# Optimization experiments

Hardware: AMD Instinct MI355X
Metric: run time of the kernel (lower is better)

The kernel has to match this reference:

```python
import jax, jax.numpy as jnp
import numpy as np

B, S, D = 2, 2048, 4096
H, KVH, HD = 32, 8, 128
MULT = 0.08838834764831845  # 1/sqrt(head_dim)
MAXV = 30.0                 # tanh soft-cap
ROPE_BASE = 10000.0


def _rope_cos_sin(position_ids, hd=HD, base=ROPE_BASE):
    inv_freq = 1.0 / (base ** (jnp.arange(0, hd, 2, dtype=jnp.float32) / hd))
    freqs = position_ids.astype(jnp.float32)[..., None] * inv_freq  # [B,S,hd/2]
    emb = jnp.concatenate([freqs, freqs], axis=-1)                  # [B,S,hd]
    return jnp.cos(emb), jnp.sin(emb)


def _rotate_half(x):
    half = x.shape[-1] // 2
    return jnp.concatenate([-x[..., half:], x[..., :half]], axis=-1)


def setup_inputs() -> dict:
    key = jax.random.key(0)
    ks = jax.random.split(key, 5)
    hidden_states = jax.random.normal(ks[0], (B, S, D), dtype=jnp.float32)
    position_ids = jnp.broadcast_to(jnp.arange(S, dtype=jnp.int64), (B, S))
    # True = masked (causal upper triangle)
    causal = jnp.triu(jnp.ones((S, S), dtype=bool), k=1)
    attention_mask = jnp.broadcast_to(causal, (B, 1, S, S))
    sc = 0.02
    q_w = jax.random.normal(ks[1], (D, H * HD), dtype=jnp.float32) * sc
    k_w = jax.random.normal(ks[2], (D, KVH * HD), dtype=jnp.float32) * sc
    v_w = jax.random.normal(ks[3], (D, KVH * HD), dtype=jnp.float32) * sc
    o_w = jax.random.normal(ks[4], (H * HD, D), dtype=jnp.float32) * sc
    return {"hidden_states": hidden_states, "position_ids": position_ids,
            "attention_mask": attention_mask, "q_w": q_w, "k_w": k_w,
            "v_w": v_w, "o_w": o_w}


def reference(hidden_states, position_ids, attention_mask, q_w, k_w, v_w, o_w):
    bsz, q_len, _ = hidden_states.shape
    q = (hidden_states @ q_w).reshape(bsz, q_len, H, HD).transpose(0, 2, 1, 3)    # [B,H,S,HD]
    k = (hidden_states @ k_w).reshape(bsz, q_len, KVH, HD).transpose(0, 2, 1, 3)  # [B,KVH,S,HD]
    v = (hidden_states @ v_w).reshape(bsz, q_len, KVH, HD).transpose(0, 2, 1, 3)

    cos, sin = _rope_cos_sin(position_ids)   # [B,S,HD]
    cos = cos[:, None]                       # [B,1,S,HD]
    sin = sin[:, None]
    q = q * cos + _rotate_half(q) * sin
    k = k * cos + _rotate_half(k) * sin

    groups = H // KVH
    k = jnp.repeat(k, groups, axis=1)        # [B,H,S,HD]
    v = jnp.repeat(v, groups, axis=1)

    scores = jnp.einsum('bhqd,bhkd->bhqk', q, k).astype(jnp.float32) * MULT
    scores = MAXV * jnp.tanh(scores / MAXV)
    scores = jnp.where(attention_mask, jnp.float32(-10000.0), scores)
    attn = jax.nn.softmax(scores, axis=-1).astype(q.dtype)

    out = jnp.einsum('bhqk,bhkd->bhqd', attn, v)       # [B,H,S,HD]
    out = out.transpose(0, 2, 1, 3).reshape(bsz, q_len, H * HD)
    return out @ o_w
```

## Files before the change

### kernel.cpp

```cpp
#include <hip/hip_runtime.h>
#include <stdint.h>

#define B_ 2
#define S_ 2048
#define D_ 4096
#define H_ 32
#define KVH_ 8
#define HD_ 128
#define GRP_ (H_/KVH_)
#define NQKV 6144
#define MULT_ 0.08838834764831845f
#define MAXV_ 30.0f

typedef __attribute__((ext_vector_type(8))) short s16x8;
typedef __attribute__((ext_vector_type(4))) float fx4;

__device__ __forceinline__ unsigned short f2bf(float f) {
  unsigned int u = __float_as_uint(f);
  u += 0x7fffu + ((u >> 16) & 1u);
  return (unsigned short)(u >> 16);
}
__device__ __forceinline__ float bf2f(unsigned short h) {
  return __uint_as_float(((unsigned int)h) << 16);
}

__device__ __forceinline__ void gld_lds16(const void* g, void* l) {
  __builtin_amdgcn_global_load_lds(
      (const __attribute__((address_space(1))) unsigned int*)g,
      (__attribute__((address_space(3))) unsigned int*)l, 16, 0, 0);
}


__global__ void k_f2bf(const float* __restrict__ src, unsigned short* __restrict__ dst, int n4) {
  int i = blockIdx.x * blockDim.x + threadIdx.x;
  int stride = gridDim.x * blockDim.x;
  for (; i < n4; i += stride) {
    float4 v = ((const float4*)src)[i];
    ushort4 o;
    o.x = f2bf(v.x); o.y = f2bf(v.y); o.z = f2bf(v.z); o.w = f2bf(v.w);
    ((ushort4*)dst)[i] = o;
  }
}

__global__ void k_transpose_w(const float* __restrict__ src, int ncols,
                              unsigned short* __restrict__ dst) {
  __shared__ float tile[32][33];
  int k0 = blockIdx.x * 32;
  int n0 = blockIdx.y * 32;
  int tx = threadIdx.x, ty = threadIdx.y;
  for (int i = 0; i < 32; i += 8)
    tile[ty + i][tx] = src[(size_t)(k0 + ty + i) * ncols + n0 + tx];
  __syncthreads();
  for (int i = 0; i < 32; i += 8)
    dst[(size_t)(n0 + ty + i) * 4096 + k0 + tx] = f2bf(tile[tx][ty + i]);
}

__global__ void k_transpose_v(const unsigned short* __restrict__ qkv,
                              unsigned short* __restrict__ vt) {
  __shared__ unsigned short tile[32][33];
  int s0 = blockIdx.x * 32;
  int d0 = blockIdx.y * 32;
  int bk = blockIdx.z;
  int b = bk / KVH_, kvh = bk % KVH_;
  int tx = threadIdx.x, ty = threadIdx.y;
  for (int i = 0; i < 32; i += 8)
    tile[ty + i][tx] = qkv[(size_t)(b*S_ + s0 + ty + i)*NQKV + 5120 + kvh*HD_ + d0 + tx];
  __syncthreads();
  for (int i = 0; i < 32; i += 8)
    vt[((size_t)bk*HD_ + d0 + ty + i)*S_ + s0 + tx] = tile[tx][ty + i];
}

__global__ void k_rope(const unsigned short* __restrict__ qkv,
                       unsigned short* __restrict__ Q, unsigned short* __restrict__ K) {
  int bs = blockIdx.x;
  int b = bs >> 11;
  int s = bs & (S_ - 1);
  __shared__ float cs[64], sn[64];
  int t = threadIdx.x;
  if (t < 64) {
    float inv = __expf(-(float)t * 0.14391156831212787f);
    float fr = (float)s * inv;
    cs[t] = cosf(fr); sn[t] = sinf(fr);
  }
  __syncthreads();
  const unsigned short* row = qkv + (size_t)bs * NQKV;
  for (int i = t; i < H_*HD_; i += 256) {
    int h = i >> 7, d = i & 127;
    float x = bf2f(row[i]);
    float x2, c, si;
    if (d < 64) { x2 = -bf2f(row[h*128 + d + 64]); c = cs[d];    si = sn[d]; }
    else        { x2 =  bf2f(row[h*128 + d - 64]); c = cs[d-64]; si = sn[d-64]; }
    Q[((size_t)(b*H_ + h)*S_ + s)*HD_ + d] = f2bf(x*c + x2*si);
  }
  for (int i = t; i < KVH_*HD_; i += 256) {
    int h = i >> 7, d = i & 127;
    float x = bf2f(row[4096 + i]);
    float x2, c, si;
    if (d < 64) { x2 = -bf2f(row[4096 + h*128 + d + 64]); c = cs[d];    si = sn[d]; }
    else        { x2 =  bf2f(row[4096 + h*128 + d - 64]); c = cs[d-64]; si = sn[d-64]; }
    K[((size_t)(b*KVH_ + h)*S_ + s)*HD_ + d] = f2bf(x*c + x2*si);
  }
}

#define BAR() asm volatile("s_barrier" ::: "memory")
#define SB0() __builtin_amdgcn_sched_barrier(0)
#define VMC6() asm volatile("s_waitcnt vmcnt(6)" ::: "memory")
#define VMC4() asm volatile("s_waitcnt vmcnt(4)" ::: "memory")


#define STG4(buf, isB, h, kt) do {                                           \
  const unsigned short* _src = (isB) ? Bt : A;                               \
  size_t _rb = (size_t)(((isB) ? bn : bm)*((isB) ? 128 : 256)                \
                        + (h)*((isB) ? 64 : 128));                           \
  _Pragma("unroll") for (int _rr = 0; _rr < ((isB) ? 1 : 2); ++_rr) {        \
    int _s = _rr*8 + wv;                                                     \
    gld_lds16(_src + (_rb + (size_t)((_s>>1)*16))*Kd                         \
                   + (size_t)((kt)*64 + (_s&1)*32) + lane_off,               \
              ldsc + (buf)*49152 + (isB)*32768                               \
                   + (h)*((isB) ? 8192 : 16384) + _s*1024);                  \
  }                                                                          \
} while (0)

#define LDA4(buf, mh) do {                                                   \
  _Pragma("unroll") for (int _i = 0; _i < 4; ++_i)                           \
  _Pragma("unroll") for (int _kk = 0; _kk < 2; ++_kk)                        \
    Afr[_i*2+_kk] = *(const s16x8*)(ldsc + (buf)*49152 + wr*16384            \
                    + ((((mh)*4+_i)*2+_kk)*1024) + aswz);                    \
} while (0)

#define LDB4(buf) do {                                                       \
  _Pragma("unroll") for (int _nf = 0; _nf < 2; ++_nf)                        \
  _Pragma("unroll") for (int _kk = 0; _kk < 2; ++_kk) {                      \
    int _r0 = wc*32 + _nf*16;                                                \
    Bfr[_nf*2+_kk] = *(const s16x8*)(ldsc + (buf)*49152 + 32768              \
                    + (_r0>>6)*8192 + ((((_r0&63)>>4)*2+_kk)*1024) + aswz);  \
  }                                                                          \
} while (0)

#define MFMA16(MH) do {                                                      \
  __builtin_amdgcn_s_setprio(1);                                            \
  _Pragma("unroll") for (int _i = 0; _i < 4; ++_i)                           \
  _Pragma("unroll") for (int _nf = 0; _nf < 2; ++_nf)                        \
  _Pragma("unroll") for (int _kk = 0; _kk < 2; ++_kk)                        \
    acc[(MH)*4+_i][_nf] = __builtin_amdgcn_mfma_f32_16x16x32_bf16(           \
        Afr[_i*2+_kk], Bfr[_nf*2+_kk], acc[(MH)*4+_i][_nf], 0, 0, 0);        \
  __builtin_amdgcn_s_setprio(0);                                            \
} while (0)

__global__ __launch_bounds__(512, 2)
void k_gemm4t(const unsigned short* __restrict__ A, const unsigned short* __restrict__ Bt,
              unsigned short* __restrict__ C, int Kdim, int N, int MB) {
  __shared__ __align__(16) char ldsbuf[147456];
  char* ldsc = ldsbuf;
  const size_t Kd = (size_t)Kdim;
  const int NT = Kdim >> 6;

  int nwg = gridDim.x;
  int flat = blockIdx.x;
  int q = nwg >> 3, r8 = nwg & 7, xcd = flat & 7, off = flat >> 3;
  int wg = (xcd < r8 ? xcd*(q+1) : r8*(q+1) + (xcd-r8)*q) + off;
  int bm = wg % MB, bn = wg / MB;

  int tid = threadIdx.x;
  int lane = tid & 63, wv = tid >> 6;
  int wr = wv >> 2, wc = wv & 3;
  int l15 = lane & 15, l4 = lane >> 4;
  const int aswz = (l15 << 6) + ((l4 << 4) ^ ((l15 & 8) ? 32 : 0));
  const size_t lane_off = (size_t)(lane >> 2) * Kd
                        + (size_t)(((lane & 3) << 3) ^ ((lane & 32) >> 1));

  fx4 acc[8][2] = {};
  s16x8 Afr[8], Bfr[4];

  STG4(0, 0, 0, 0); STG4(0, 0, 1, 0); STG4(0, 1, 0, 0); STG4(0, 1, 1, 0);
  STG4(1, 0, 0, 1); STG4(1, 0, 1, 1); STG4(1, 1, 0, 1); STG4(1, 1, 1, 1);
  VMC6();
  BAR();

  int r0 = 0, r1 = 1, r2 = 2;
  for (int t = 0; t < NT; ++t) {
    int tp2 = t + 2; if (tp2 >= NT) tp2 -= NT;
    LDA4(r0, 0); LDB4(r0);
    STG4(r2, 0, 0, tp2); STG4(r2, 0, 1, tp2);
    BAR();
    MFMA16(0);
    SB0(); BAR();
    LDA4(r0, 1);
    STG4(r2, 1, 0, tp2); STG4(r2, 1, 1, tp2);
    BAR();
    MFMA16(1);
    SB0(); VMC6(); BAR();
    int tmp = r0; r0 = r1; r1 = r2; r2 = tmp;
  }

  int m0 = bm*256 + wr*128 + l4*4;
#pragma unroll
  for (int af = 0; af < 8; ++af)
#pragma unroll
    for (int nf = 0; nf < 2; ++nf)
#pragma unroll
      for (int r = 0; r < 4; ++r) {
        int m = m0 + af*16 + r;
        int n = bn*128 + wc*32 + nf*16 + l15;
        C[(size_t)m*N + n] = f2bf(acc[af][nf][r]);
      }
}


#define STAGE(buf, isB, h, kt) do {                                          \
  const unsigned short* _src = (isB) ? Bt : A;                               \
  size_t _rb = (size_t)(((isB) ? bn : bm)*256 + (h)*128);                    \
  _Pragma("unroll") for (int _rr = 0; _rr < 2; ++_rr) {                      \
    int _s = _rr*8 + wv;                                                     \
    gld_lds16(_src + (_rb + (size_t)((_s>>1)*16))*Kd                         \
                   + (size_t)((kt)*64 + (_s&1)*32) + lane_off,               \
              ldsc + (buf)*65536 + (isB)*32768 + (h)*16384 + _s*1024);       \
  }                                                                          \
} while (0)

#define LDA(dst, buf, mh) do {                                               \
  _Pragma("unroll") for (int _i = 0; _i < 4; ++_i)                           \
  _Pragma("unroll") for (int _kk = 0; _kk < 2; ++_kk)                        \
    dst[_i*2+_kk] = *(const s16x8*)(ldsc + (buf)*65536 + wr*16384            \
                    + ((((mh)*4+_i)*2+_kk)*1024) + aswz);                    \
} while (0)

#define LDB(dst, buf, nh) do {                                               \
  _Pragma("unroll") for (int _j = 0; _j < 2; ++_j)                           \
  _Pragma("unroll") for (int _kk = 0; _kk < 2; ++_kk)                        \
    dst[_j*2+_kk] = *(const s16x8*)(ldsc + (buf)*65536 + 32768               \
                    + (wc>>1)*16384                                          \
                    + ((((wc&1)*4+(nh)*2+_j)*2+_kk)*1024) + aswz);           \
} while (0)

#define MFMA_Q(Aa, Bb, MH, NH) do {                                          \
  __builtin_amdgcn_s_setprio(1);                                            \
  _Pragma("unroll") for (int _i = 0; _i < 4; ++_i)                           \
  _Pragma("unroll") for (int _j = 0; _j < 2; ++_j)                           \
  _Pragma("unroll") for (int _kk = 0; _kk < 2; ++_kk)                        \
    acc[(MH)*4+_i][(NH)*2+_j] = __builtin_amdgcn_mfma_f32_16x16x32_bf16(     \
        Aa[_i*2+_kk], Bb[_j*2+_kk], acc[(MH)*4+_i][(NH)*2+_j], 0, 0, 0);     \
  __builtin_amdgcn_s_setprio(0);                                            \
} while (0)

__global__ __launch_bounds__(512, 2)
void k_gemm8(const unsigned short* __restrict__ A, const unsigned short* __restrict__ Bt,
             float* __restrict__ C, int Kdim, int N, int MB) {
  __shared__ __align__(16) char ldsbuf[131072];
  char* ldsc = ldsbuf;
  const size_t Kd = (size_t)Kdim;
  const int NT = Kdim >> 6;

  int nwg = gridDim.x;
  int flat = blockIdx.x;
  int q = nwg >> 3, r8 = nwg & 7, xcd = flat & 7, off = flat >> 3;
  int wg = (xcd < r8 ? xcd*(q+1) : r8*(q+1) + (xcd-r8)*q) + off;
  int bm = wg % MB, bn = wg / MB;

  int tid = threadIdx.x;
  int lane = tid & 63, wv = tid >> 6;
  int wr = wv >> 2, wc = wv & 3;
  int l15 = lane & 15, l4 = lane >> 4;
  const int aswz = (l15 << 6) + ((l4 << 4) ^ ((l15 & 8) ? 32 : 0));
  const size_t lane_off = (size_t)(lane >> 2) * Kd
                        + (size_t)(((lane & 3) << 3) ^ ((lane & 32) >> 1));

  fx4 acc[8][4] = {};
  s16x8 Afr[8], B0fr[4], B1fr[4];

  STAGE(0, 0, 0, 0); STAGE(0, 0, 1, 0);
  STAGE(0, 1, 0, 0); STAGE(0, 1, 1, 0);
  STAGE(1, 1, 0, 1); STAGE(1, 1, 1, 1);
  VMC4();
  BAR();

  for (int t2 = 0; t2 < NT; t2 += 2) {
    int tb1 = t2 + 1;
    int tn0 = t2 + 2; if (tn0 >= NT) tn0 -= NT;
    int tn1 = t2 + 3; if (tn1 >= NT) tn1 -= NT;
    LDA(Afr, 0, 0); LDB(B0fr, 0, 0);
    STAGE(1, 0, 0, tb1);
    BAR();
    MFMA_Q(Afr, B0fr, 0, 0);
    SB0(); BAR();
    LDB(B1fr, 0, 1);
    STAGE(1, 0, 1, tb1);
    BAR();
    MFMA_Q(Afr, B1fr, 0, 1);
    SB0(); BAR();
    LDA(Afr, 0, 1);
    STAGE(0, 1, 0, tn0);
    BAR();
    MFMA_Q(Afr, B1fr, 1, 1);
    SB0(); BAR();
    STAGE(0, 1, 1, tn0);
    BAR();
    MFMA_Q(Afr, B0fr, 1, 0);
    SB0(); VMC4(); BAR();
    LDA(Afr, 1, 0); LDB(B0fr, 1, 0);
    STAGE(0, 0, 0, tn0);
    BAR();
    MFMA_Q(Afr, B0fr, 0, 0);
    SB0(); BAR();
    LDB(B1fr, 1, 1);
    STAGE(0, 0, 1, tn0);
    BAR();
    MFMA_Q(Afr, B1fr, 0, 1);
    SB0(); BAR();
    LDA(Afr, 1, 1);
    STAGE(1, 1, 0, tn1);
    BAR();
    MFMA_Q(Afr, B1fr, 1, 1);
    SB0(); BAR();
    STAGE(1, 1, 1, tn1);
    BAR();
    MFMA_Q(Afr, B0fr, 1, 0);
    SB0(); VMC4(); BAR();
  }

  int m0 = bm*256 + wr*128 + l4*4;
#pragma unroll
  for (int mf = 0; mf < 8; ++mf)
#pragma unroll
    for (int nf = 0; nf < 4; ++nf)
#pragma unroll
      for (int r = 0; r < 4; ++r) {
        int m = m0 + mf*16 + r;
        int n = bn*256 + (wc>>1)*128 + ((wc&1)*4 + nf)*16 + l15;
        C[(size_t)m*N + n] = acc[mf][nf][r];
      }
}


__global__ __launch_bounds__(256)
void k_attn8(const unsigned short* __restrict__ Q, const unsigned short* __restrict__ K,
             const unsigned short* __restrict__ Vt, unsigned short* __restrict__ Aout) {
  __shared__ unsigned short k_lds[2][32*128];
  __shared__ unsigned short v_lds[2][128*32];
  const float C1 = MULT_ * 2.0f * 1.4426950408889634f / MAXV_;
  const float C3 = 2.0f * MAXV_ * 1.4426950408889634f;
  int tpair = blockIdx.x;
  int bh = blockIdx.y;
  int b = bh >> 5, h = bh & 31;
  int kvh = h >> 2;
  int tid = threadIdx.x, lane = tid & 63, wv = tid >> 6;
  int l15 = lane & 15, l4 = lane >> 4;
  const unsigned short* Qb = Q + (size_t)bh * S_ * HD_;
  const unsigned short* Kb = K + (size_t)(b*KVH_ + kvh) * S_ * HD_;
  const unsigned short* Vb = Vt + (size_t)(b*KVH_ + kvh) * HD_ * S_;

  s16x8 ones;
#pragma unroll
  for (int i = 0; i < 8; ++i) ones[i] = (short)0x3F80;

#define STAGE_KV32(bufi, kb32) do {                                          \
  _Pragma("unroll") for (int _it = 0; _it < 2; ++_it) {                      \
    int _c = _it*256 + tid;                                                  \
    int _kr = _c >> 4;                                                       \
    int _kd = ((_c & 15) ^ (_kr & 7)) * 8;                                   \
    gld_lds16(&Kb[(size_t)((kb32) + _kr)*HD_ + _kd],                         \
              &k_lds[bufi][_it*2048 + wv*512]);                              \
    int _vd = _c >> 2;                                                       \
    int _vk = ((_c & 3) ^ (_vd & 3)) * 8;                                    \
    gld_lds16(&Vb[(size_t)_vd*S_ + (kb32) + _vk],                            \
              &v_lds[bufi][_it*2048 + wv*512]);                              \
  }                                                                          \
} while (0)

  for (int sp = 0; sp < 2; ++sp) {
    int strip = sp ? (31 - tpair) : tpair;
    int q0 = strip * 64;
    int qbase = q0 + wv * 16;
    int qr = qbase + l15;
    s16x8 bq[4];
#pragma unroll
    for (int kb = 0; kb < 4; ++kb)
      bq[kb] = *(const s16x8*)&Qb[(size_t)qr*HD_ + kb*32 + l4*8];
    fx4 oacc[8] = {};
    fx4 osum = {};
    int nt_full = qbase >> 5;
    int nt = (q0 >> 5) + 2;

    auto body = [&](int bufi, int kbase, bool domask) {
      fx4 sst[2] = {};
      __builtin_amdgcn_s_setprio(1);
#pragma unroll
      for (int nb = 0; nb < 2; ++nb)
#pragma unroll
        for (int kb = 0; kb < 4; ++kb) {
          s16x8 kf = *(const s16x8*)&k_lds[bufi][(nb*16 + l15)*128 + (((kb*4 + l4) ^ (l15 & 7)) * 8)];
          sst[nb] = __builtin_amdgcn_mfma_f32_16x16x32_bf16(kf, bq[kb], sst[nb], 0, 0, 0);
        }
      __builtin_amdgcn_s_setprio(0);
      uint32_t w[4];
#pragma unroll
      for (int nb = 0; nb < 2; ++nb) {
        float pv[4];
#pragma unroll
        for (int r = 0; r < 4; ++r) {
          float sraw = sst[nb][r];
          float e2p = __builtin_amdgcn_exp2f(sraw * C1);
          float p = __builtin_amdgcn_exp2f(-C3 * __builtin_amdgcn_rcpf(1.f + e2p));
          if (domask) {
            int kk = kbase + nb*16 + l4*4 + r;
            p = (kk <= qr) ? p : 0.f;
          }
          pv[r] = p;
        }
        w[nb*2]   = __builtin_amdgcn_perm(__float_as_uint(pv[1]), __float_as_uint(pv[0]), 0x07060302u);
        w[nb*2+1] = __builtin_amdgcn_perm(__float_as_uint(pv[3]), __float_as_uint(pv[2]), 0x07060302u);
      }
      uint32_t a0x = __shfl_xor((int)w[0], 16), a1x = __shfl_xor((int)w[1], 16);
      uint32_t b0x = __shfl_xor((int)w[2], 16), b1x = __shfl_xor((int)w[3], 16);
      bool up = (l4 & 1);
      uint32_t VA0 = up ? a0x : w[0], VA1 = up ? a1x : w[1];
      uint32_t VA2 = up ? w[0] : a0x, VA3 = up ? w[1] : a1x;
      uint32_t VB0 = up ? b0x : w[2], VB1 = up ? b1x : w[3];
      uint32_t VB2 = up ? w[2] : b0x, VB3 = up ? w[3] : b1x;
      bool lowh = (l4 < 2);
      uint32_t X0 = lowh ? VB0 : VA0, X1 = lowh ? VB1 : VA1;
      uint32_t X2 = lowh ? VB2 : VA2, X3 = lowh ? VB3 : VA3;
      uint32_t Y0 = __shfl_xor((int)X0, 32), Y1 = __shfl_xor((int)X1, 32);
      uint32_t Y2 = __shfl_xor((int)X2, 32), Y3 = __shfl_xor((int)X3, 32);
      union { uint32_t u[4]; s16x8 v; } tw;
      tw.u[0] = (l4 == 0) ? VA0 : (l4 == 3) ? VB0 : Y0;
      tw.u[1] = (l4 == 0) ? VA1 : (l4 == 3) ? VB1 : Y1;
      tw.u[2] = (l4 == 0) ? VA2 : (l4 == 3) ? VB2 : Y2;
      tw.u[3] = (l4 == 0) ? VA3 : (l4 == 3) ? VB3 : Y3;
      s16x8 pf = tw.v;
      __builtin_amdgcn_s_setprio(1);
      osum = __builtin_amdgcn_mfma_f32_16x16x32_bf16(ones, pf, osum, 0, 0, 0);
#pragma unroll
      for (int db = 0; db < 8; ++db) {
        int d = db*16 + l15;
        s16x8 vf = *(const s16x8*)&v_lds[bufi][d*32 + ((l4 ^ (d & 3)) * 8)];
        oacc[db] = __builtin_amdgcn_mfma_f32_16x16x32_bf16(vf, pf, oacc[db], 0, 0, 0);
      }
      __builtin_amdgcn_s_setprio(0);
    };

    STAGE_KV32(0, 0);
    __syncthreads();
    for (int t = 0; t < nt; ++t) {
      int bufi = t & 1;
      if (t + 1 < nt) STAGE_KV32(bufi^1, (t+1)*32);
      if (t < nt_full)       body(bufi, t*32, false);
      else if (t == nt_full) body(bufi, t*32, true);
      __syncthreads();
    }

    float rn = __builtin_amdgcn_rcpf(osum[0]);
#pragma unroll
    for (int db = 0; db < 8; ++db) {
      ushort4 o;
      o.x = f2bf(oacc[db][0] * rn);
      o.y = f2bf(oacc[db][1] * rn);
      o.z = f2bf(oacc[db][2] * rn);
      o.w = f2bf(oacc[db][3] * rn);
      *(ushort4*)&Aout[(size_t)(b*S_ + qr)*4096 + h*HD_ + db*16 + l4*4] = o;
    }
  }
#undef STAGE_KV32
}


extern "C" void kernel_launch(void* const* d_in, const int* in_sizes, int n_in,
                              void* d_out, int out_size, void* d_ws, size_t ws_size,
                              hipStream_t stream) {
  (void)in_sizes; (void)n_in; (void)out_size; (void)ws_size;
  const float* hidden = (const float*)d_in[0];
  const float* q_w = (const float*)d_in[3];
  const float* k_w = (const float*)d_in[4];
  const float* v_w = (const float*)d_in[5];
  const float* o_w = (const float*)d_in[6];
  char* ws = (char*)d_ws;
  unsigned short* hidden_bf = (unsigned short*)(ws + 0);
  unsigned short* qkv_wt    = (unsigned short*)(ws + 33554432);
  unsigned short* o_wt      = (unsigned short*)(ws + 83886080);
  unsigned short* qkv       = (unsigned short*)(ws + 117440512);
  unsigned short* Qb        = (unsigned short*)(ws + 167772160);
  unsigned short* Kb        = (unsigned short*)(ws + 201326592);
  unsigned short* Vt        = (unsigned short*)(ws + 209715200);
  unsigned short* attn_out  = (unsigned short*)(ws + 218103808);

  dim3 tb(32, 8);
  k_f2bf<<<2048, 256, 0, stream>>>(hidden, hidden_bf, (B_*S_*D_)/4);
  k_transpose_w<<<dim3(128, 128), tb, 0, stream>>>(q_w, 4096, qkv_wt);
  k_transpose_w<<<dim3(128, 32),  tb, 0, stream>>>(k_w, 1024, qkv_wt + (size_t)4096*4096);
  k_transpose_w<<<dim3(128, 32),  tb, 0, stream>>>(v_w, 1024, qkv_wt + (size_t)5120*4096);
  k_transpose_w<<<dim3(128, 128), tb, 0, stream>>>(o_w, 4096, o_wt);
  k_gemm4t<<<dim3(16*48), 512, 0, stream>>>(hidden_bf, qkv_wt, qkv, D_, NQKV, 16);
  k_rope<<<B_*S_, 256, 0, stream>>>(qkv, Qb, Kb);
  k_transpose_v<<<dim3(S_/32, HD_/32, B_*KVH_), tb, 0, stream>>>(qkv, Vt);
  k_attn8<<<dim3(16, 64), 256, 0, stream>>>(Qb, Kb, Vt, attn_out);
  k_gemm8<<<dim3(16*16), 512, 0, stream>>>(attn_out, o_wt, (float*)d_out, D_, D_, 16);
}
```

Baseline: 589.2 us.

## Widen QKV GEMM tile to 256x192 with double-buffered LDS staging

Replaces the 256x128 QKV projection GEMM with a 256x192 tile, so each wave computes 48 columns and the grid drops from 768 to 512 workgroups. The triple-buffered pipeline with a two-tile prefetch and partial vmcnt waits becomes a double-buffered one that issues all next-tile loads up front and waits for vmcnt(0) at the end of each iteration. The wider tile is meant to raise arithmetic intensity and cut the number of tiles so 512 blocks fit the CU count better. The cost is more accumulator registers and a shallower prefetch that may expose memory latency.

```diff
diff --git a/kernel.cpp b/kernel.cpp
--- a/kernel.cpp
+++ b/kernel.cpp
@@ -104,53 +104,60 @@
 
 #define BAR() asm volatile("s_barrier" ::: "memory")
 #define SB0() __builtin_amdgcn_sched_barrier(0)
-#define VMC6() asm volatile("s_waitcnt vmcnt(6)" ::: "memory")
+#define VMC0() asm volatile("s_waitcnt vmcnt(0)" ::: "memory")
 #define VMC4() asm volatile("s_waitcnt vmcnt(4)" ::: "memory")
 
 
-#define STG4(buf, isB, h, kt) do {                                           \
-  const unsigned short* _src = (isB) ? Bt : A;                               \
-  size_t _rb = (size_t)(((isB) ? bn : bm)*((isB) ? 128 : 256)                \
-                        + (h)*((isB) ? 64 : 128));                           \
-  _Pragma("unroll") for (int _rr = 0; _rr < ((isB) ? 1 : 2); ++_rr) {        \
+#define PB192 57344
+
+#define STGA192(buf, h, kt) do {                                             \
+  size_t _rb = (size_t)(bm*256 + (h)*128);                                   \
+  _Pragma("unroll") for (int _rr = 0; _rr < 2; ++_rr) {                      \
     int _s = _rr*8 + wv;                                                     \
-    gld_lds16(_src + (_rb + (size_t)((_s>>1)*16))*Kd                         \
-                   + (size_t)((kt)*64 + (_s&1)*32) + lane_off,               \
-              ldsc + (buf)*49152 + (isB)*32768                               \
-                   + (h)*((isB) ? 8192 : 16384) + _s*1024);                  \
+    gld_lds16(A + (_rb + (size_t)((_s>>1)*16))*Kd                            \
+                + (size_t)((kt)*64 + (_s&1)*32) + lane_off,                  \
+              ldsc + (buf)*PB192 + (h)*16384 + _s*1024);                     \
   }                                                                          \
 } while (0)
 
-#define LDA4(buf, mh) do {                                                   \
+#define STGB192(buf, c, kt) do {                                             \
+  size_t _rb = (size_t)(bn*192 + (c)*64);                                    \
+  {                                                                          \
+    int _s = wv;                                                             \
+    gld_lds16(Bt + (_rb + (size_t)((_s>>1)*16))*Kd                           \
+                 + (size_t)((kt)*64 + (_s&1)*32) + lane_off,                 \
+              ldsc + (buf)*PB192 + 32768 + (c)*8192 + _s*1024);              \
+  }                                                                          \
+} while (0)
+
+#define LDA192(buf, mh) do {                                                 \
   _Pragma("unroll") for (int _i = 0; _i < 4; ++_i)                           \
   _Pragma("unroll") for (int _kk = 0; _kk < 2; ++_kk)                        \
-    Afr[_i*2+_kk] = *(const s16x8*)(ldsc + (buf)*49152 + wr*16384            \
+    Afr[_i*2+_kk] = *(const s16x8*)(ldsc + (buf)*PB192 + wr*16384            \
                     + ((((mh)*4+_i)*2+_kk)*1024) + aswz);                    \
 } while (0)
 
-#define LDB4(buf) do {                                                       \
-  _Pragma("unroll") for (int _nf = 0; _nf < 2; ++_nf)                        \
-  _Pragma("unroll") for (int _kk = 0; _kk < 2; ++_kk) {                      \
-    int _r0 = wc*32 + _nf*16;                                                \
-    Bfr[_nf*2+_kk] = *(const s16x8*)(ldsc + (buf)*49152 + 32768              \
-                    + (_r0>>6)*8192 + ((((_r0&63)>>4)*2+_kk)*1024) + aswz);  \
-  }                                                                          \
-} while (0)
-
-#define MFMA16(MH) do {                                                      \
+#define LDB192(buf) do {                                                     \
+  _Pragma("unroll") for (int _j = 0; _j < 3; ++_j)                           \
+  _Pragma("unroll") for (int _kk = 0; _kk < 2; ++_kk)                        \
+    Bfr[_j*2+_kk] = *(const s16x8*)(ldsc + (buf)*PB192 + 32768               \
+                    + (((wc*3+_j)*2+_kk)*1024) + aswz);                      \
+} while (0)
+
+#define MFMA24(MH) do {                                                      \
   __builtin_amdgcn_s_setprio(1);                                            \
   _Pragma("unroll") for (int _i = 0; _i < 4; ++_i)                           \
-  _Pragma("unroll") for (int _nf = 0; _nf < 2; ++_nf)                        \
+  _Pragma("unroll") for (int _j = 0; _j < 3; ++_j)                           \
   _Pragma("unroll") for (int _kk = 0; _kk < 2; ++_kk)                        \
-    acc[(MH)*4+_i][_nf] = __builtin_amdgcn_mfma_f32_16x16x32_bf16(           \
-        Afr[_i*2+_kk], Bfr[_nf*2+_kk], acc[(MH)*4+_i][_nf], 0, 0, 0);        \
+    acc[(MH)*4+_i][_j] = __builtin_amdgcn_mfma_f32_16x16x32_bf16(            \
+        Afr[_i*2+_kk], Bfr[_j*2+_kk], acc[(MH)*4+_i][_j], 0, 0, 0);          \
   __builtin_amdgcn_s_setprio(0);                                            \
 } while (0)
 
 __global__ __launch_bounds__(512, 2)
-void k_gemm4t(const unsigned short* __restrict__ A, const unsigned short* __restrict__ Bt,
-              unsigned short* __restrict__ C, int Kdim, int N, int MB) {
-  __shared__ __align__(16) char ldsbuf[147456];
+void k_gemm192(const unsigned short* __restrict__ A, const unsigned short* __restrict__ Bt,
+               unsigned short* __restrict__ C, int Kdim, int N, int MB) {
+  __shared__ __align__(16) char ldsbuf[2*PB192];
   char* ldsc = ldsbuf;
   const size_t Kd = (size_t)Kdim;
   const int NT = Kdim >> 6;
@@ -169,40 +176,39 @@
   const size_t lane_off = (size_t)(lane >> 2) * Kd
                         + (size_t)(((lane & 3) << 3) ^ ((lane & 32) >> 1));
 
-  fx4 acc[8][2] = {};
-  s16x8 Afr[8], Bfr[4];
-
-  STG4(0, 0, 0, 0); STG4(0, 0, 1, 0); STG4(0, 1, 0, 0); STG4(0, 1, 1, 0);
-  STG4(1, 0, 0, 1); STG4(1, 0, 1, 1); STG4(1, 1, 0, 1); STG4(1, 1, 1, 1);
-  VMC6();
+  fx4 acc[8][3] = {};
+  s16x8 Afr[8], Bfr[6];
+
+  STGB192(0, 0, 0); STGB192(0, 1, 0); STGB192(0, 2, 0);
+  STGA192(0, 0, 0); STGA192(0, 1, 0);
+  VMC0();
   BAR();
 
-  int r0 = 0, r1 = 1, r2 = 2;
   for (int t = 0; t < NT; ++t) {
-    int tp2 = t + 2; if (tp2 >= NT) tp2 -= NT;
-    LDA4(r0, 0); LDB4(r0);
-    STG4(r2, 0, 0, tp2); STG4(r2, 0, 1, tp2);
-    BAR();
-    MFMA16(0);
-    SB0(); BAR();
-    LDA4(r0, 1);
-    STG4(r2, 1, 0, tp2); STG4(r2, 1, 1, tp2);
-    BAR();
-    MFMA16(1);
-    SB0(); VMC6(); BAR();
-    int tmp = r0; r0 = r1; r1 = r2; r2 = tmp;
+    int p = t & 1;
+    int tp1 = t + 1; if (tp1 >= NT) tp1 -= NT;
+    LDA192(p, 0); LDB192(p);
+    STGB192(p^1, 0, tp1); STGB192(p^1, 1, tp1); STGB192(p^1, 2, tp1);
+    STGA192(p^1, 0, tp1); STGA192(p^1, 1, tp1);
+    BAR();
+    MFMA24(0);
+    SB0(); BAR();
+    LDA192(p, 1);
+    BAR();
+    MFMA24(1);
+    SB0(); VMC0(); BAR();
   }
 
   int m0 = bm*256 + wr*128 + l4*4;
 #pragma unroll
   for (int af = 0; af < 8; ++af)
 #pragma unroll
-    for (int nf = 0; nf < 2; ++nf)
+    for (int j = 0; j < 3; ++j)
 #pragma unroll
       for (int r = 0; r < 4; ++r) {
         int m = m0 + af*16 + r;
-        int n = bn*128 + wc*32 + nf*16 + l15;
-        C[(size_t)m*N + n] = f2bf(acc[af][nf][r]);
+        int n = bn*192 + wc*48 + j*16 + l15;
+        C[(size_t)m*N + n] = f2bf(acc[af][j][r]);
       }
 }
 
@@ -489,7 +495,7 @@
   k_transpose_w<<<dim3(128, 32),  tb, 0, stream>>>(k_w, 1024, qkv_wt + (size_t)4096*4096);
   k_transpose_w<<<dim3(128, 32),  tb, 0, stream>>>(v_w, 1024, qkv_wt + (size_t)5120*4096);
   k_transpose_w<<<dim3(128, 128), tb, 0, stream>>>(o_w, 4096, o_wt);
-  k_gemm4t<<<dim3(16*48), 512, 0, stream>>>(hidden_bf, qkv_wt, qkv, D_, NQKV, 16);
+  k_gemm192<<<dim3(16*32), 512, 0, stream>>>(hidden_bf, qkv_wt, qkv, D_, NQKV, 16);
   k_rope<<<B_*S_, 256, 0, stream>>>(qkv, Qb, Kb);
   k_transpose_v<<<dim3(S_/32, HD_/32, B_*KVH_), tb, 0, stream>>>(qkv, Vt);
   k_attn8<<<dim3(16, 64), 256, 0, stream>>>(Qb, Kb, Vt, attn_out);
```

Result: slower. 606.6 us (+3.0%).
